# Performance work log

Hardware: AMD Instinct MI355X
Metric: run time of the kernel (lower is better)

Reference implementation:

```python
import jax, jax.numpy as jnp
import numpy as np

N_NODES = 50000
N_EDGES = 800000
D = 64
N_REL = 16


def setup_inputs() -> dict:
    key = jax.random.key(0)
    ks = jax.random.split(key, 8)
    return {
        "nfeat": jax.random.normal(ks[0], (N_NODES, D), dtype=jnp.float32),
        "efeat": jax.random.normal(ks[1], (N_EDGES, D), dtype=jnp.float32),
        "relation_W": jax.random.normal(ks[2], (N_REL, D, D), dtype=jnp.float32) * (1.0 / np.sqrt(D)),
        "W1": jax.random.normal(ks[3], (D, D), dtype=jnp.float32) * (1.0 / np.sqrt(D)),
        "W2": jax.random.normal(ks[4], (D, D), dtype=jnp.float32) * (1.0 / np.sqrt(D)),
        "src": jax.random.randint(ks[5], (N_EDGES,), 0, N_NODES, dtype=jnp.int32),
        "dst": jax.random.randint(ks[6], (N_EDGES,), 0, N_NODES, dtype=jnp.int32),
        "etype": jax.random.randint(ks[7], (N_EDGES,), 0, N_REL, dtype=jnp.int32),
    }


def _leaky_relu(x, slope=0.01):
    return jnp.where(x >= 0, x, slope * x)


def reference(nfeat, efeat, relation_W, W1, W2, src, dst, etype):
    N, Din = nfeat.shape
    R, _, Dr = relation_W.shape
    # W_r h for every (relation, node) pair, then gather per-edge.
    # Mathematically identical to per-edge bmm_maybe_select, but avoids the
    # (E, Din, Dr) per-edge weight materialization.
    proj = jnp.einsum('nd,rde->rne', nfeat, relation_W).reshape(R * N, Dr)  # (R*N, Dr)
    flat_src = etype * N + src
    flat_dst = etype * N + dst
    t_r = proj[flat_src]  # (E, Dr) == W_r h_t
    h_r = proj[flat_dst]  # (E, Dr) == W_r h_h
    # att = (W_r h_t)^T tanh(W_r h_h + e_r)
    att = jnp.sum(t_r * jnp.tanh(h_r + efeat), axis=-1)  # (E,)
    # edge softmax grouped by destination node
    seg_max = jax.ops.segment_max(att, dst, num_segments=N)  # (N,)
    ex = jnp.exp(att - seg_max[dst])
    denom = jax.ops.segment_sum(ex, dst, num_segments=N)  # (N,)
    a = ex / denom[dst]  # (E,)
    # u_mul_e + sum scatter aggregation
    h_neighbor = jax.ops.segment_sum(nfeat[src] * a[:, None], dst, num_segments=N)  # (N, Din)
    # Bi-interaction residual
    out = _leaky_relu((nfeat + h_neighbor) @ W1) + _leaky_relu((nfeat * h_neighbor) @ W2)
    return (h_neighbor, out)
```

## Files before the change

kernel.cpp:

```cpp
#include <hip/hip_runtime.h>
#include <math.h>


#define DIM 64
#define PA 72

typedef _Float16 half8 __attribute__((ext_vector_type(8)));
typedef float f32x4 __attribute__((ext_vector_type(4)));
typedef unsigned int u32x4 __attribute__((ext_vector_type(4)));

__device__ __forceinline__ float4 f4zero() { return make_float4(0.f, 0.f, 0.f, 0.f); }

__device__ __forceinline__ unsigned short f2bf(float x) {
    unsigned u = __float_as_uint(x);
    u += 0x7FFFu + ((u >> 16) & 1u);
    return (unsigned short)(u >> 16);
}

__device__ __forceinline__ float fast_tanh(float x) {
    float ex = __expf(2.0f * x);
    return 1.0f - 2.0f / (ex + 1.0f);
}

__device__ __forceinline__ void bf8up(u32x4 u, float* f) {
    f[0] = __uint_as_float(u[0] << 16);
    f[1] = __uint_as_float(u[0] & 0xFFFF0000u);
    f[2] = __uint_as_float(u[1] << 16);
    f[3] = __uint_as_float(u[1] & 0xFFFF0000u);
    f[4] = __uint_as_float(u[2] << 16);
    f[5] = __uint_as_float(u[2] & 0xFFFF0000u);
    f[6] = __uint_as_float(u[3] << 16);
    f[7] = __uint_as_float(u[3] & 0xFFFF0000u);
}

__global__ __launch_bounds__(256) void k_proj(const float* __restrict__ nfeat,
                                              const float* __restrict__ relW,
                                              unsigned short* __restrict__ proj,
                                              int N, int R) {
    __shared__ _Float16 shA[64 * PA];
    __shared__ _Float16 shB[64 * PA];
    unsigned short* shSt = (unsigned short*)shA;

    const int tx = threadIdx.x;
    const int n0 = blockIdx.x * 64;
    const int rpb = R >> 2;
    const int rb = blockIdx.y * rpb;

    const float4* nf4 = (const float4*)(nfeat + (size_t)n0 * DIM);
#pragma unroll
    for (int i = 0; i < 4; ++i) {
        int idx = tx + 256 * i;
        int row = idx >> 4, c = idx & 15;
        float4 v = (n0 + row < N) ? nf4[idx] : f4zero();
        _Float16* p = &shA[row * PA + c * 4];
        p[0] = (_Float16)v.x; p[1] = (_Float16)v.y;
        p[2] = (_Float16)v.z; p[3] = (_Float16)v.w;
    }
    __syncthreads();

    const int w = tx >> 6;
    const int lane = tx & 63;
    const int lm = lane & 15;
    const int lq = lane >> 4;
    const int m0 = w * 16;

    half8 a0 = *(const half8*)&shA[(m0 + lm) * PA + 0 * 32 + lq * 8];
    half8 a1 = *(const half8*)&shA[(m0 + lm) * PA + 1 * 32 + lq * 8];

    for (int rr = 0; rr < rpb; ++rr) {
        const int r = rb + rr;
        __syncthreads();
        const float4* Wr4 = (const float4*)(relW + (size_t)r * DIM * DIM);
#pragma unroll
        for (int i = 0; i < 4; ++i) {
            int idx = tx + 256 * i;
            int d = idx >> 4, c = (idx & 15) * 4;
            float4 v = Wr4[idx];
            shB[(c + 0) * PA + d] = (_Float16)v.x;
            shB[(c + 1) * PA + d] = (_Float16)v.y;
            shB[(c + 2) * PA + d] = (_Float16)v.z;
            shB[(c + 3) * PA + d] = (_Float16)v.w;
        }
        __syncthreads();

        f32x4 acc[4];
#pragma unroll
        for (int ct = 0; ct < 4; ++ct) {
            half8 b0 = *(const half8*)&shB[(ct * 16 + lm) * PA + 0 * 32 + lq * 8];
            half8 b1 = *(const half8*)&shB[(ct * 16 + lm) * PA + 1 * 32 + lq * 8];
            f32x4 c = {0.f, 0.f, 0.f, 0.f};
            c = __builtin_amdgcn_mfma_f32_16x16x32_f16(a0, b0, c, 0, 0, 0);
            c = __builtin_amdgcn_mfma_f32_16x16x32_f16(a1, b1, c, 0, 0, 0);
            acc[ct] = c;
        }

#pragma unroll
        for (int ct = 0; ct < 4; ++ct) {
#pragma unroll
            for (int i = 0; i < 4; ++i) {
                int row = m0 + lq * 4 + i;
                int col = ct * 16 + lm;
                shSt[row * PA + col] = f2bf(acc[ct][i]);
            }
        }
        __syncthreads();

        unsigned short* projR = proj + ((size_t)r * N + n0) * DIM;
#pragma unroll
        for (int k = 0; k < 2; ++k) {
            int chunk = tx + k * 256;
            int row = chunk >> 3, cc = chunk & 7;
            uint4 v = *(const uint4*)&shSt[row * PA + cc * 8];
            if (n0 + row < N)
                *(uint4*)&projR[(size_t)row * DIM + cc * 8] = v;
        }
    }
}

__global__ __launch_bounds__(256) void k_hist(const int* __restrict__ dst,
                                              int* __restrict__ deg,
                                              int* __restrict__ rank, int E) {
    int e = blockIdx.x * 256 + threadIdx.x;
    if (e < E) rank[e] = atomicAdd(&deg[dst[e]], 1);
}

__global__ __launch_bounds__(256) void k_scan1(const int* __restrict__ deg,
                                               int* __restrict__ epart,
                                               int* __restrict__ bsum, int N) {
    __shared__ int sh[256];
    int i = blockIdx.x * 256 + threadIdx.x;
    int t = threadIdx.x;
    int v = (i < N) ? deg[i] : 0;
    sh[t] = v;
    __syncthreads();
#pragma unroll
    for (int d = 1; d < 256; d <<= 1) {
        int o = (t >= d) ? sh[t - d] : 0;
        __syncthreads();
        sh[t] += o;
        __syncthreads();
    }
    if (i < N) epart[i] = sh[t] - v;
    if (t == 255) bsum[blockIdx.x] = sh[255];
}

__global__ __launch_bounds__(1024) void k_scan2(const int* __restrict__ epart,
                                                const int* __restrict__ bsum,
                                                int nb,
                                                int* __restrict__ off,
                                                int N, int E) {
    __shared__ int bx[256];
    int t = threadIdx.x;
    int v = 0;
    if (t < 256) {
        v = (t < nb) ? bsum[t] : 0;
        bx[t] = v;
    }
    __syncthreads();
#pragma unroll
    for (int d = 1; d < 256; d <<= 1) {
        int o = 0;
        if (t < 256 && t >= d) o = bx[t - d];
        __syncthreads();
        if (t < 256) bx[t] += o;
        __syncthreads();
    }
    if (t < 256) bx[t] -= v;
    __syncthreads();
    for (int i = t; i < N; i += 1024)
        off[i] = epart[i] + bx[i >> 8];
    if (t == 0) off[N] = E;
}

__global__ __launch_bounds__(256) void k_att(const unsigned short* __restrict__ proj,
                                             const float* __restrict__ efeat,
                                             const int* __restrict__ src,
                                             const int* __restrict__ dst,
                                             const int* __restrict__ etype,
                                             const int* __restrict__ rank,
                                             const int* __restrict__ off,
                                             float* __restrict__ att_s,
                                             int* __restrict__ src_s,
                                             int N, int E) {
    int t = blockIdx.x * 256 + threadIdx.x;
    int e = t >> 3;
    int sub = t & 7;
    if (e >= E) return;
    int s = src[e], d = dst[e], r = etype[e];

    const u32x4* tp = (const u32x4*)(proj + ((size_t)((unsigned)(r * N + s))) * DIM) + sub;
    const u32x4* hp = (const u32x4*)(proj + ((size_t)((unsigned)(r * N + d))) * DIM) + sub;
    const f32x4* ef = (const f32x4*)(efeat + (size_t)e * DIM) + sub * 2;

    u32x4 tu = *tp;
    u32x4 hu = *hp;
    f32x4 efa = __builtin_nontemporal_load(ef);
    f32x4 efb = __builtin_nontemporal_load(ef + 1);

    float tf[8], hf[8];
    bf8up(tu, tf);
    bf8up(hu, hf);
    float ev[8] = {efa[0], efa[1], efa[2], efa[3], efb[0], efb[1], efb[2], efb[3]};

    float dotv = 0.f;
#pragma unroll
    for (int i = 0; i < 8; ++i)
        dotv = fmaf(tf[i], fast_tanh(hf[i] + ev[i]), dotv);

    dotv += __shfl_xor(dotv, 1);
    dotv += __shfl_xor(dotv, 2);
    dotv += __shfl_xor(dotv, 4);

    int p = off[d] + rank[e];
    if (sub == 0) att_s[p] = dotv;
    if (sub == 1) src_s[p] = s;
}

__global__ __launch_bounds__(256) void k_agg(const float* __restrict__ att_s,
                                             const int* __restrict__ src_s,
                                             const float* __restrict__ nfeat,
                                             const int* __restrict__ off,
                                             float* __restrict__ hn, int N) {
    const int node = blockIdx.x * 4 + (threadIdx.x >> 6);
    if (node >= N) return;
    const int lane = threadIdx.x & 63;
    const int qw = lane >> 4;
    const int ql = lane & 15;

    const int jb = off[node];
    const int je = off[node + 1];

    float m = -INFINITY;
    for (int j0 = jb; j0 < je; j0 += 64) {
        int j = j0 + lane;
        float a = (j < je) ? att_s[j] : -INFINITY;
        m = fmaxf(m, a);
    }
#pragma unroll
    for (int ms = 32; ms; ms >>= 1) m = fmaxf(m, __shfl_xor(m, ms));

    float pl = 0.f;
    f32x4 acc = {0.f, 0.f, 0.f, 0.f};
    for (int j0 = jb; j0 < je; j0 += 64) {
        int j = j0 + lane;
        int cnt = min(64, je - j0);
        float a = (j < je) ? att_s[j] : -INFINITY;
        float p = __expf(a - m);
        int s = (j < je) ? src_s[j] : 0;
        pl += p;

        int jj = 0;
        for (; jj + 15 < cnt; jj += 16) {
            float pj[4]; int sj[4]; f32x4 x[4];
#pragma unroll
            for (int u = 0; u < 4; ++u) {
                int eidx = jj + u * 4 + qw;
                pj[u] = __shfl(p, eidx);
                sj[u] = __shfl(s, eidx);
            }
#pragma unroll
            for (int u = 0; u < 4; ++u)
                x[u] = *(const f32x4*)&nfeat[(size_t)sj[u] * DIM + ql * 4];
#pragma unroll
            for (int u = 0; u < 4; ++u) {
                acc[0] = fmaf(pj[u], x[u][0], acc[0]);
                acc[1] = fmaf(pj[u], x[u][1], acc[1]);
                acc[2] = fmaf(pj[u], x[u][2], acc[2]);
                acc[3] = fmaf(pj[u], x[u][3], acc[3]);
            }
        }
        for (; jj < cnt; jj += 4) {
            int eidx = jj + qw;
            int ec = (eidx < cnt) ? eidx : (cnt - 1);
            float pj = __shfl(p, ec);
            int sj = __shfl(s, ec);
            if (eidx < cnt) {
                f32x4 x = *(const f32x4*)&nfeat[(size_t)sj * DIM + ql * 4];
                acc[0] = fmaf(pj, x[0], acc[0]);
                acc[1] = fmaf(pj, x[1], acc[1]);
                acc[2] = fmaf(pj, x[2], acc[2]);
                acc[3] = fmaf(pj, x[3], acc[3]);
            }
        }
    }
#pragma unroll
    for (int ms = 32; ms; ms >>= 1) pl += __shfl_xor(pl, ms);

#pragma unroll
    for (int c = 0; c < 4; ++c) {
        acc[c] += __shfl_xor(acc[c], 16);
        acc[c] += __shfl_xor(acc[c], 32);
    }

    const float inv = (je > jb) ? 1.0f / pl : 0.f;
    if (qw == 0) {
        f32x4 hv = {acc[0] * inv, acc[1] * inv, acc[2] * inv, acc[3] * inv};
        *(f32x4*)&hn[(size_t)node * DIM + ql * 4] = hv;
    }
}

__global__ __launch_bounds__(256) void k_bi(const float* __restrict__ nfeat,
                                            const float* __restrict__ hn,
                                            const float* __restrict__ W1,
                                            const float* __restrict__ W2,
                                            float* __restrict__ out, int N) {
    __shared__ _Float16 shMem[4 * 64 * PA];
    _Float16* shA1 = shMem;
    _Float16* shA2 = shMem + 64 * PA;
    _Float16* shB1 = shMem + 2 * 64 * PA;
    _Float16* shB2 = shMem + 3 * 64 * PA;

    const int tx = threadIdx.x;
    const int n0 = blockIdx.x * 64;

    const float4* nf4 = (const float4*)(nfeat + (size_t)n0 * DIM);
    const float4* hn4 = (const float4*)(hn + (size_t)n0 * DIM);
#pragma unroll
    for (int i = 0; i < 4; ++i) {
        int idx = tx + 256 * i;
        int row = idx >> 4, c = idx & 15;
        bool ok = (n0 + row < N);
        float4 a = ok ? nf4[idx] : f4zero();
        float4 b = ok ? hn4[idx] : f4zero();
        _Float16* p1 = &shA1[row * PA + c * 4];
        _Float16* p2 = &shA2[row * PA + c * 4];
        p1[0] = (_Float16)(a.x + b.x); p2[0] = (_Float16)(a.x * b.x);
        p1[1] = (_Float16)(a.y + b.y); p2[1] = (_Float16)(a.y * b.y);
        p1[2] = (_Float16)(a.z + b.z); p2[2] = (_Float16)(a.z * b.z);
        p1[3] = (_Float16)(a.w + b.w); p2[3] = (_Float16)(a.w * b.w);
    }
    const float4* w14 = (const float4*)W1;
    const float4* w24 = (const float4*)W2;
#pragma unroll
    for (int i = 0; i < 4; ++i) {
        int idx = tx + 256 * i;
        int k = idx >> 4, c = (idx & 15) * 4;
        float4 v = w14[idx];
        shB1[(c + 0) * PA + k] = (_Float16)v.x;
        shB1[(c + 1) * PA + k] = (_Float16)v.y;
        shB1[(c + 2) * PA + k] = (_Float16)v.z;
        shB1[(c + 3) * PA + k] = (_Float16)v.w;
        float4 u = w24[idx];
        shB2[(c + 0) * PA + k] = (_Float16)u.x;
        shB2[(c + 1) * PA + k] = (_Float16)u.y;
        shB2[(c + 2) * PA + k] = (_Float16)u.z;
        shB2[(c + 3) * PA + k] = (_Float16)u.w;
    }
    __syncthreads();

    const int w = tx >> 6;
    const int lane = tx & 63;
    const int lm = lane & 15;
    const int lq = lane >> 4;
    const int m0 = w * 16;

    half8 a10 = *(const half8*)&shA1[(m0 + lm) * PA + 0 * 32 + lq * 8];
    half8 a11 = *(const half8*)&shA1[(m0 + lm) * PA + 1 * 32 + lq * 8];
    half8 a20 = *(const half8*)&shA2[(m0 + lm) * PA + 0 * 32 + lq * 8];
    half8 a21 = *(const half8*)&shA2[(m0 + lm) * PA + 1 * 32 + lq * 8];

    f32x4 res[4];
#pragma unroll
    for (int ct = 0; ct < 4; ++ct) {
        half8 b10 = *(const half8*)&shB1[(ct * 16 + lm) * PA + 0 * 32 + lq * 8];
        half8 b11 = *(const half8*)&shB1[(ct * 16 + lm) * PA + 1 * 32 + lq * 8];
        half8 b20 = *(const half8*)&shB2[(ct * 16 + lm) * PA + 0 * 32 + lq * 8];
        half8 b21 = *(const half8*)&shB2[(ct * 16 + lm) * PA + 1 * 32 + lq * 8];
        f32x4 c1 = {0.f, 0.f, 0.f, 0.f};
        f32x4 c2 = {0.f, 0.f, 0.f, 0.f};
        c1 = __builtin_amdgcn_mfma_f32_16x16x32_f16(a10, b10, c1, 0, 0, 0);
        c1 = __builtin_amdgcn_mfma_f32_16x16x32_f16(a11, b11, c1, 0, 0, 0);
        c2 = __builtin_amdgcn_mfma_f32_16x16x32_f16(a20, b20, c2, 0, 0, 0);
        c2 = __builtin_amdgcn_mfma_f32_16x16x32_f16(a21, b21, c2, 0, 0, 0);
#pragma unroll
        for (int i = 0; i < 4; ++i) {
            float o1 = c1[i], o2 = c2[i];
            res[ct][i] = (o1 >= 0.f ? o1 : 0.01f * o1) + (o2 >= 0.f ? o2 : 0.01f * o2);
        }
    }

    __syncthreads();
    float* shSt = (float*)shMem;
#pragma unroll
    for (int ct = 0; ct < 4; ++ct)
#pragma unroll
        for (int i = 0; i < 4; ++i)
            shSt[(m0 + lq * 4 + i) * 68 + ct * 16 + lm] = res[ct][i];
    __syncthreads();

    float* outp = out + (size_t)n0 * DIM;
#pragma unroll
    for (int k = 0; k < 4; ++k) {
        int idx = tx + 256 * k;
        int row = idx >> 4, cc = idx & 15;
        if (n0 + row < N) {
            float4 v = *(const float4*)&shSt[row * 68 + cc * 4];
            *(float4*)&outp[(size_t)row * DIM + cc * 4] = v;
        }
    }
}

extern "C" void kernel_launch(void* const* d_in, const int* in_sizes, int n_in,
                              void* d_out, int out_size, void* d_ws, size_t ws_size,
                              hipStream_t stream) {
    const float* nfeat = (const float*)d_in[0];
    const float* efeat = (const float*)d_in[1];
    const float* relW  = (const float*)d_in[2];
    const float* W1    = (const float*)d_in[3];
    const float* W2    = (const float*)d_in[4];
    const int* src   = (const int*)d_in[5];
    const int* dst   = (const int*)d_in[6];
    const int* etype = (const int*)d_in[7];

    const int N = in_sizes[0] / DIM;
    const int E = in_sizes[5];
    const int R = in_sizes[2] / (DIM * DIM);
    const int NB = (N + 255) / 256;

    float* out = (float*)d_out;
    float* hn  = out;
    float* bi  = out + (size_t)N * DIM;

    unsigned short* proj = (unsigned short*)d_ws;
    size_t projElems = (size_t)R * N * DIM;
    int* deg    = (int*)(proj + projElems);
    int* off    = deg + N;
    int* epart  = off + (N + 1);
    int* bsum   = epart + N;
    int* rank   = bsum + 256;
    int* src_s  = rank + E;
    float* att_s = (float*)(src_s + E);

    (void)hipMemsetAsync(deg, 0, (size_t)N * sizeof(int), stream);

    k_hist<<<(E + 255) / 256, 256, 0, stream>>>(dst, deg, rank, E);
    k_scan1<<<NB, 256, 0, stream>>>(deg, epart, bsum, N);
    k_scan2<<<1, 1024, 0, stream>>>(epart, bsum, NB, off, N, E);

    dim3 gProj((N + 63) / 64, 4);
    k_proj<<<gProj, 256, 0, stream>>>(nfeat, relW, proj, N, R);

    k_att<<<((size_t)E * 8 + 255) / 256, 256, 0, stream>>>(proj, efeat, src, dst, etype,
                                                           rank, off, att_s, src_s, N, E);

    k_agg<<<(N + 3) / 4, 256, 0, stream>>>(att_s, src_s, nfeat, off, hn, N);

    k_bi<<<(N + 63) / 64, 256, 0, stream>>>(nfeat, hn, W1, W2, bi, N);
}
```

Before: 468.7 us.

## Compute per-edge relation projections on the fly instead of materializing R×N projection

Removes the precomputed bf16 projection table for every (relation, node) pair. Edges are instead bucketed by relation type with a per-block histogram, scan and fill, and each 64-edge tile gathers source and destination node features and multiplies them by that relation's weight using MFMA. This avoids writing and randomly re-reading a large projection buffer, and it replaces the bf16 storage with fp16 compute. In exchange it adds three small sorting kernels, duplicates the matmul work per edge rather than per node, and reads efeat in a strided per-element pattern.

```diff
diff --git a/kernel.cpp b/kernel.cpp
--- a/kernel.cpp
+++ b/kernel.cpp
@@ -7,114 +7,12 @@
 
 typedef _Float16 half8 __attribute__((ext_vector_type(8)));
 typedef float f32x4 __attribute__((ext_vector_type(4)));
-typedef unsigned int u32x4 __attribute__((ext_vector_type(4)));
 
 __device__ __forceinline__ float4 f4zero() { return make_float4(0.f, 0.f, 0.f, 0.f); }
-
-__device__ __forceinline__ unsigned short f2bf(float x) {
-    unsigned u = __float_as_uint(x);
-    u += 0x7FFFu + ((u >> 16) & 1u);
-    return (unsigned short)(u >> 16);
-}
 
 __device__ __forceinline__ float fast_tanh(float x) {
     float ex = __expf(2.0f * x);
     return 1.0f - 2.0f / (ex + 1.0f);
-}
-
-__device__ __forceinline__ void bf8up(u32x4 u, float* f) {
-    f[0] = __uint_as_float(u[0] << 16);
-    f[1] = __uint_as_float(u[0] & 0xFFFF0000u);
-    f[2] = __uint_as_float(u[1] << 16);
-    f[3] = __uint_as_float(u[1] & 0xFFFF0000u);
-    f[4] = __uint_as_float(u[2] << 16);
-    f[5] = __uint_as_float(u[2] & 0xFFFF0000u);
-    f[6] = __uint_as_float(u[3] << 16);
-    f[7] = __uint_as_float(u[3] & 0xFFFF0000u);
-}
-
-__global__ __launch_bounds__(256) void k_proj(const float* __restrict__ nfeat,
-                                              const float* __restrict__ relW,
-                                              unsigned short* __restrict__ proj,
-                                              int N, int R) {
-    __shared__ _Float16 shA[64 * PA];
-    __shared__ _Float16 shB[64 * PA];
-    unsigned short* shSt = (unsigned short*)shA;
-
-    const int tx = threadIdx.x;
-    const int n0 = blockIdx.x * 64;
-    const int rpb = R >> 2;
-    const int rb = blockIdx.y * rpb;
-
-    const float4* nf4 = (const float4*)(nfeat + (size_t)n0 * DIM);
-#pragma unroll
-    for (int i = 0; i < 4; ++i) {
-        int idx = tx + 256 * i;
-        int row = idx >> 4, c = idx & 15;
-        float4 v = (n0 + row < N) ? nf4[idx] : f4zero();
-        _Float16* p = &shA[row * PA + c * 4];
-        p[0] = (_Float16)v.x; p[1] = (_Float16)v.y;
-        p[2] = (_Float16)v.z; p[3] = (_Float16)v.w;
-    }
-    __syncthreads();
-
-    const int w = tx >> 6;
-    const int lane = tx & 63;
-    const int lm = lane & 15;
-    const int lq = lane >> 4;
-    const int m0 = w * 16;
-
-    half8 a0 = *(const half8*)&shA[(m0 + lm) * PA + 0 * 32 + lq * 8];
-    half8 a1 = *(const half8*)&shA[(m0 + lm) * PA + 1 * 32 + lq * 8];
-
-    for (int rr = 0; rr < rpb; ++rr) {
-        const int r = rb + rr;
-        __syncthreads();
-        const float4* Wr4 = (const float4*)(relW + (size_t)r * DIM * DIM);
-#pragma unroll
-        for (int i = 0; i < 4; ++i) {
-            int idx = tx + 256 * i;
-            int d = idx >> 4, c = (idx & 15) * 4;
-            float4 v = Wr4[idx];
-            shB[(c + 0) * PA + d] = (_Float16)v.x;
-            shB[(c + 1) * PA + d] = (_Float16)v.y;
-            shB[(c + 2) * PA + d] = (_Float16)v.z;
-            shB[(c + 3) * PA + d] = (_Float16)v.w;
-        }
-        __syncthreads();
-
-        f32x4 acc[4];
-#pragma unroll
-        for (int ct = 0; ct < 4; ++ct) {
-            half8 b0 = *(const half8*)&shB[(ct * 16 + lm) * PA + 0 * 32 + lq * 8];
-            half8 b1 = *(const half8*)&shB[(ct * 16 + lm) * PA + 1 * 32 + lq * 8];
-            f32x4 c = {0.f, 0.f, 0.f, 0.f};
-            c = __builtin_amdgcn_mfma_f32_16x16x32_f16(a0, b0, c, 0, 0, 0);
-            c = __builtin_amdgcn_mfma_f32_16x16x32_f16(a1, b1, c, 0, 0, 0);
-            acc[ct] = c;
-        }
-
-#pragma unroll
-        for (int ct = 0; ct < 4; ++ct) {
-#pragma unroll
-            for (int i = 0; i < 4; ++i) {
-                int row = m0 + lq * 4 + i;
-                int col = ct * 16 + lm;
-                shSt[row * PA + col] = f2bf(acc[ct][i]);
-            }
-        }
-        __syncthreads();
-
-        unsigned short* projR = proj + ((size_t)r * N + n0) * DIM;
-#pragma unroll
-        for (int k = 0; k < 2; ++k) {
-            int chunk = tx + k * 256;
-            int row = chunk >> 3, cc = chunk & 7;
-            uint4 v = *(const uint4*)&shSt[row * PA + cc * 8];
-            if (n0 + row < N)
-                *(uint4*)&projR[(size_t)row * DIM + cc * 8] = v;
-        }
-    }
 }
 
 __global__ __launch_bounds__(256) void k_hist(const int* __restrict__ dst,
@@ -172,48 +70,205 @@
     if (t == 0) off[N] = E;
 }
 
-__global__ __launch_bounds__(256) void k_att(const unsigned short* __restrict__ proj,
-                                             const float* __restrict__ efeat,
-                                             const int* __restrict__ src,
-                                             const int* __restrict__ dst,
-                                             const int* __restrict__ etype,
-                                             const int* __restrict__ rank,
-                                             const int* __restrict__ off,
-                                             float* __restrict__ att_s,
-                                             int* __restrict__ src_s,
-                                             int N, int E) {
-    int t = blockIdx.x * 256 + threadIdx.x;
-    int e = t >> 3;
-    int sub = t & 7;
-    if (e >= E) return;
-    int s = src[e], d = dst[e], r = etype[e];
-
-    const u32x4* tp = (const u32x4*)(proj + ((size_t)((unsigned)(r * N + s))) * DIM) + sub;
-    const u32x4* hp = (const u32x4*)(proj + ((size_t)((unsigned)(r * N + d))) * DIM) + sub;
-    const f32x4* ef = (const f32x4*)(efeat + (size_t)e * DIM) + sub * 2;
-
-    u32x4 tu = *tp;
-    u32x4 hu = *hp;
-    f32x4 efa = __builtin_nontemporal_load(ef);
-    f32x4 efb = __builtin_nontemporal_load(ef + 1);
-
-    float tf[8], hf[8];
-    bf8up(tu, tf);
-    bf8up(hu, hf);
-    float ev[8] = {efa[0], efa[1], efa[2], efa[3], efb[0], efb[1], efb[2], efb[3]};
-
-    float dotv = 0.f;
-#pragma unroll
-    for (int i = 0; i < 8; ++i)
-        dotv = fmaf(tf[i], fast_tanh(hf[i] + ev[i]), dotv);
-
-    dotv += __shfl_xor(dotv, 1);
-    dotv += __shfl_xor(dotv, 2);
-    dotv += __shfl_xor(dotv, 4);
-
-    int p = off[d] + rank[e];
-    if (sub == 0) att_s[p] = dotv;
-    if (sub == 1) src_s[p] = s;
+__global__ __launch_bounds__(256) void k_thist(const int* __restrict__ etype,
+                                               int* __restrict__ bh,
+                                               int nbe, int E) {
+    __shared__ int h[16];
+    const int tx = threadIdx.x, b = blockIdx.x;
+    if (tx < 16) h[tx] = 0;
+    __syncthreads();
+    int e = b * 256 + tx;
+    if (e < E) atomicAdd(&h[etype[e]], 1);
+    __syncthreads();
+    if (tx < 16) bh[(size_t)tx * nbe + b] = h[tx];
+}
+
+__global__ __launch_bounds__(1024) void k_tscan(int* __restrict__ bh, int nbe,
+                                                int* __restrict__ hdr) {
+    __shared__ int cntS[16];
+    __shared__ int tstartS[16];
+    const int tx = threadIdx.x;
+    const int w = tx >> 6;
+    const int lane = tx & 63;
+    int* row = bh + (size_t)w * nbe;
+
+    int run = 0;
+    for (int i0 = 0; i0 < nbe; i0 += 64) {
+        int idx = i0 + lane;
+        int v = (idx < nbe) ? row[idx] : 0;
+        int incl = v;
+#pragma unroll
+        for (int d = 1; d < 64; d <<= 1) {
+            int o = __shfl_up(incl, d);
+            if (lane >= d) incl += o;
+        }
+        if (idx < nbe) row[idx] = run + (incl - v);
+        run += __shfl(incl, 63);
+    }
+    if (lane == 0) cntS[w] = run;
+    __syncthreads();
+    if (tx == 0) {
+        int ts = 0, tp = 0;
+        for (int r = 0; r < 16; ++r) {
+            tstartS[r] = ts;
+            hdr[r] = ts;
+            hdr[17 + r] = tp;
+            ts += cntS[r];
+            tp += (cntS[r] + 63) >> 6;
+        }
+        hdr[16] = ts;
+        hdr[33] = tp;
+    }
+    __syncthreads();
+    const int t0 = tstartS[w];
+    for (int i0 = 0; i0 < nbe; i0 += 64) {
+        int idx = i0 + lane;
+        if (idx < nbe) row[idx] += t0;
+    }
+}
+
+__global__ __launch_bounds__(256) void k_tfill(const int* __restrict__ src,
+                                               const int* __restrict__ dst,
+                                               const int* __restrict__ etype,
+                                               const int* __restrict__ rank,
+                                               const int* __restrict__ off,
+                                               const int* __restrict__ bh, int nbe,
+                                               int* __restrict__ sS,
+                                               int* __restrict__ dS,
+                                               int* __restrict__ pS,
+                                               int* __restrict__ eS, int E) {
+    __shared__ int h[16];
+    const int tx = threadIdx.x, b = blockIdx.x;
+    if (tx < 16) h[tx] = 0;
+    __syncthreads();
+    int e = b * 256 + tx;
+    if (e < E) {
+        int r = etype[e];
+        int mr = atomicAdd(&h[r], 1);
+        int slot = bh[(size_t)r * nbe + b] + mr;
+        int d = dst[e];
+        sS[slot] = src[e];
+        dS[slot] = d;
+        pS[slot] = off[d] + rank[e];
+        eS[slot] = e;
+    }
+}
+
+__global__ __launch_bounds__(256) void k_attE(const float* __restrict__ nfeat,
+                                              const float* __restrict__ efeat,
+                                              const float* __restrict__ relW,
+                                              const int* __restrict__ hdr,
+                                              const int* __restrict__ sS,
+                                              const int* __restrict__ dS,
+                                              const int* __restrict__ pS,
+                                              const int* __restrict__ eS,
+                                              float* __restrict__ att_s,
+                                              int* __restrict__ src_s) {
+    __shared__ _Float16 shS[64 * PA];
+    __shared__ _Float16 shD[64 * PA];
+    __shared__ _Float16 shB[64 * PA];
+
+    const int bid = blockIdx.x;
+    if (bid >= hdr[33]) return;
+    int r = 0;
+    while (r < 15 && bid >= hdr[17 + r + 1]) ++r;
+    const int e0 = hdr[r] + ((bid - hdr[17 + r]) << 6);
+    const int cnt = min(64, hdr[r + 1] - e0);
+
+    const int tx = threadIdx.x;
+
+    const float4* Wr4 = (const float4*)(relW + (size_t)r * DIM * DIM);
+#pragma unroll
+    for (int i = 0; i < 4; ++i) {
+        int idx = tx + 256 * i;
+        int d = idx >> 4, c = (idx & 15) * 4;
+        float4 v = Wr4[idx];
+        shB[(c + 0) * PA + d] = (_Float16)v.x;
+        shB[(c + 1) * PA + d] = (_Float16)v.y;
+        shB[(c + 2) * PA + d] = (_Float16)v.z;
+        shB[(c + 3) * PA + d] = (_Float16)v.w;
+    }
+#pragma unroll
+    for (int i = 0; i < 4; ++i) {
+        int idx = tx + 256 * i;
+        int row = idx >> 4, c = idx & 15;
+        bool ok = (row < cnt);
+        int sn = ok ? sS[e0 + row] : 0;
+        int dn = ok ? dS[e0 + row] : 0;
+        float4 a = ok ? *(const float4*)&nfeat[(size_t)sn * DIM + c * 4] : f4zero();
+        float4 b = ok ? *(const float4*)&nfeat[(size_t)dn * DIM + c * 4] : f4zero();
+        _Float16* p1 = &shS[row * PA + c * 4];
+        _Float16* p2 = &shD[row * PA + c * 4];
+        p1[0] = (_Float16)a.x; p1[1] = (_Float16)a.y;
+        p1[2] = (_Float16)a.z; p1[3] = (_Float16)a.w;
+        p2[0] = (_Float16)b.x; p2[1] = (_Float16)b.y;
+        p2[2] = (_Float16)b.z; p2[3] = (_Float16)b.w;
+    }
+    __syncthreads();
+
+    const int w = tx >> 6;
+    const int lane = tx & 63;
+    const int lm = lane & 15;
+    const int lq = lane >> 4;
+    const int m0 = w * 16;
+
+    half8 as0 = *(const half8*)&shS[(m0 + lm) * PA + 0 * 32 + lq * 8];
+    half8 as1 = *(const half8*)&shS[(m0 + lm) * PA + 1 * 32 + lq * 8];
+    half8 ad0 = *(const half8*)&shD[(m0 + lm) * PA + 0 * 32 + lq * 8];
+    half8 ad1 = *(const half8*)&shD[(m0 + lm) * PA + 1 * 32 + lq * 8];
+
+    f32x4 T[4], H[4];
+#pragma unroll
+    for (int ct = 0; ct < 4; ++ct) {
+        half8 b0 = *(const half8*)&shB[(ct * 16 + lm) * PA + 0 * 32 + lq * 8];
+        half8 b1 = *(const half8*)&shB[(ct * 16 + lm) * PA + 1 * 32 + lq * 8];
+        f32x4 c1 = {0.f, 0.f, 0.f, 0.f};
+        f32x4 c2 = {0.f, 0.f, 0.f, 0.f};
+        c1 = __builtin_amdgcn_mfma_f32_16x16x32_f16(as0, b0, c1, 0, 0, 0);
+        c1 = __builtin_amdgcn_mfma_f32_16x16x32_f16(as1, b1, c1, 0, 0, 0);
+        c2 = __builtin_amdgcn_mfma_f32_16x16x32_f16(ad0, b0, c2, 0, 0, 0);
+        c2 = __builtin_amdgcn_mfma_f32_16x16x32_f16(ad1, b1, c2, 0, 0, 0);
+        T[ct] = c1;
+        H[ct] = c2;
+    }
+
+    int ei[4];
+#pragma unroll
+    for (int i = 0; i < 4; ++i) {
+        int row = m0 + lq * 4 + i;
+        ei[i] = (row < cnt) ? eS[e0 + row] : -1;
+    }
+
+    float part[4] = {0.f, 0.f, 0.f, 0.f};
+#pragma unroll
+    for (int ct = 0; ct < 4; ++ct) {
+        int col = ct * 16 + lm;
+#pragma unroll
+        for (int i = 0; i < 4; ++i) {
+            float ef = (ei[i] >= 0)
+                ? __builtin_nontemporal_load(&efeat[(size_t)ei[i] * DIM + col])
+                : 0.f;
+            part[i] = fmaf(T[ct][i], fast_tanh(H[ct][i] + ef), part[i]);
+        }
+    }
+#pragma unroll
+    for (int i = 0; i < 4; ++i) {
+        part[i] += __shfl_xor(part[i], 1);
+        part[i] += __shfl_xor(part[i], 2);
+        part[i] += __shfl_xor(part[i], 4);
+        part[i] += __shfl_xor(part[i], 8);
+    }
+    if (lm == 0) {
+#pragma unroll
+        for (int i = 0; i < 4; ++i) {
+            int row = m0 + lq * 4 + i;
+            if (row < cnt) {
+                int p = pS[e0 + row];
+                att_s[p] = part[i];
+                src_s[p] = sS[e0 + row];
+            }
+        }
+    }
 }
 
 __global__ __launch_bounds__(256) void k_agg(const float* __restrict__ att_s,
@@ -414,34 +469,41 @@
 
     const int N = in_sizes[0] / DIM;
     const int E = in_sizes[5];
-    const int R = in_sizes[2] / (DIM * DIM);
     const int NB = (N + 255) / 256;
+    const int NBE = (E + 255) / 256;
 
     float* out = (float*)d_out;
     float* hn  = out;
     float* bi  = out + (size_t)N * DIM;
 
-    unsigned short* proj = (unsigned short*)d_ws;
-    size_t projElems = (size_t)R * N * DIM;
-    int* deg    = (int*)(proj + projElems);
+    int* deg    = (int*)d_ws;
     int* off    = deg + N;
     int* epart  = off + (N + 1);
     int* bsum   = epart + N;
     int* rank   = bsum + 256;
     int* src_s  = rank + E;
     float* att_s = (float*)(src_s + E);
+    int* bh     = (int*)(att_s + E);
+    int* hdr    = bh + (size_t)16 * NBE;
+    int* sS     = hdr + 64;
+    int* dS     = sS + E;
+    int* pS     = dS + E;
+    int* eS     = pS + E;
 
     (void)hipMemsetAsync(deg, 0, (size_t)N * sizeof(int), stream);
 
-    k_hist<<<(E + 255) / 256, 256, 0, stream>>>(dst, deg, rank, E);
+    k_hist<<<NBE, 256, 0, stream>>>(dst, deg, rank, E);
     k_scan1<<<NB, 256, 0, stream>>>(deg, epart, bsum, N);
     k_scan2<<<1, 1024, 0, stream>>>(epart, bsum, NB, off, N, E);
 
-    dim3 gProj((N + 63) / 64, 4);
-    k_proj<<<gProj, 256, 0, stream>>>(nfeat, relW, proj, N, R);
-
-    k_att<<<((size_t)E * 8 + 255) / 256, 256, 0, stream>>>(proj, efeat, src, dst, etype,
-                                                           rank, off, att_s, src_s, N, E);
+    k_thist<<<NBE, 256, 0, stream>>>(etype, bh, NBE, E);
+    k_tscan<<<1, 1024, 0, stream>>>(bh, NBE, hdr);
+    k_tfill<<<NBE, 256, 0, stream>>>(src, dst, etype, rank, off, bh, NBE,
+                                     sS, dS, pS, eS, E);
+
+    const int nTiles = (E + 63) / 64 + 16;
+    k_attE<<<nTiles, 256, 0, stream>>>(nfeat, efeat, relW, hdr,
+                                       sS, dS, pS, eS, att_s, src_s);
 
     k_agg<<<(N + 3) / 4, 256, 0, stream>>>(att_s, src_s, nfeat, off, hn, N);
 
```

Measured after the change: 548.4 us. +17.0%, slower.
